# Optimization experiments

Hardware: AMD Instinct MI355X
Metric: run time of the kernel (lower is better)

Reference implementation:

```python
import jax, jax.numpy as jnp
import numpy as np

B, S, E, H = 4, 2048, 1024, 16
Dh = E // H
EPS = 1e-5


def setup_inputs() -> dict:
    key = jax.random.key(0)
    ks = jax.random.split(key, 16)
    w = lambda k, shp: jax.random.normal(k, shp, dtype=jnp.float32) * 0.02
    return {
        "x": jax.random.normal(ks[0], (B, S, E), dtype=jnp.float32),
        "Wq": w(ks[1], (E, E)), "bq": jnp.zeros((E,), jnp.float32),
        "Wk": w(ks[2], (E, E)), "bk": jnp.zeros((E,), jnp.float32),
        "Wv": w(ks[3], (E, E)), "bv": jnp.zeros((E,), jnp.float32),
        "Wo": w(ks[4], (E, E)), "bo": jnp.zeros((E,), jnp.float32),
        "an1_a": jnp.ones((1, S, 1), jnp.float32),
        "an1_b": jnp.zeros((1, S, 1), jnp.float32),
        "W1": w(ks[5], (2 * E, E)), "b1": jnp.zeros((2 * E,), jnp.float32),
        "W2": w(ks[6], (E, 2 * E)), "b2": jnp.zeros((E,), jnp.float32),
        "an2_a": jnp.ones((1, S, 1), jnp.float32),
        "an2_b": jnp.zeros((1, S, 1), jnp.float32),
    }


def adaptive_norm(x, a, b):
    # AdaptiveNorm((1, N_s, 1)): normalize over embedding dim, per-position affine.
    mu = jnp.mean(x, axis=-1, keepdims=True)
    var = jnp.mean(jnp.square(x - mu), axis=-1, keepdims=True)
    return a * (x - mu) * jax.lax.rsqrt(var + EPS) + b


def reference(x, Wq, bq, Wk, bk, Wv, bv, Wo, bo, an1_a, an1_b, W1, b1, W2, b2, an2_a, an2_b):
    scale = 1.0 / np.sqrt(E / H)
    # QKV projections -> (B, S, H, Dh)
    q = (x @ Wq.T + bq).reshape(B, S, H, Dh)
    k = (x @ Wk.T + bk).reshape(B, S, H, Dh)
    v = (x @ Wv.T + bv).reshape(B, S, H, Dh)
    # scaled dot-product attention (materializes B,H,S,S like the original)
    scores = jnp.einsum("bshd,bthd->bhst", q, k) * scale
    probs = jax.nn.softmax(scores, axis=-1)
    attn = jnp.einsum("bhst,bthd->bshd", probs, v).reshape(B, S, E)
    attn = attn @ Wo.T + bo
    # residual + adaptive norm (dropout is identity in eval mode)
    h = adaptive_norm(attn + x, an1_a, an1_b)
    ff = jax.nn.relu(h @ W1.T + b1) @ W2.T + b2
    out = adaptive_norm(ff + h, an2_a, an2_b)
    return out
```

## Files before the change

kernel.cpp:

```cpp
#include <hip/hip_runtime.h>


typedef __attribute__((ext_vector_type(8))) short s16x8;
typedef __attribute__((ext_vector_type(4))) short s16x4;
typedef __attribute__((ext_vector_type(4))) unsigned short u16x4;
typedef __attribute__((ext_vector_type(4))) float f32x4;

__device__ __forceinline__ float bf2f(unsigned short u) {
  unsigned int v = ((unsigned int)u) << 16;
  return __builtin_bit_cast(float, v);
}
__device__ __forceinline__ unsigned short f2bf(float f) {
  unsigned int u = __builtin_bit_cast(unsigned int, f);
  u += 0x7fffu + ((u >> 16) & 1u);
  return (unsigned short)(u >> 16);
}
__device__ __forceinline__ unsigned int pkbf_trunc(float f0, float f1) {
  return __builtin_amdgcn_perm(__builtin_bit_cast(unsigned int, f1),
                               __builtin_bit_cast(unsigned int, f0), 0x07060302u);
}
__device__ __forceinline__ f32x4 mfma16(s16x8 a, s16x8 b, f32x4 c) {
  return __builtin_amdgcn_mfma_f32_16x16x32_bf16(a, b, c, 0, 0, 0);
}
__device__ __forceinline__ void gl2lds16(const unsigned short* g, unsigned short* l) {
  __builtin_amdgcn_global_load_lds(
      (const __attribute__((address_space(1))) unsigned int*)(g),
      (__attribute__((address_space(3))) unsigned int*)(l), 16, 0, 0);
}

__global__ void detect_dtype(const unsigned int* __restrict__ x, int* __restrict__ flag) {
  const int tid = threadIdx.x;
  int cnt = 0;
  for (int i = tid; i < 2048; i += 256) {
    const unsigned e = (x[i] >> 7) & 0xFF;
    cnt += (e >= 100 && e <= 150) ? 1 : 0;
  }
#pragma unroll
  for (int off = 32; off >= 1; off >>= 1) cnt += __shfl_xor(cnt, off);
  __shared__ int red[4];
  if ((tid & 63) == 0) red[tid >> 6] = cnt;
  __syncthreads();
  if (tid == 0) *flag = ((red[0] + red[1] + red[2] + red[3]) > 1536) ? 1 : 0;
}

struct CvtArgs {
  const void* src[17];
  unsigned short* dst[17];
  int cum4[18];
};

__global__ __launch_bounds__(256) void cvt_all(CvtArgs a, const int* __restrict__ flag, int total4) {
  const int i = blockIdx.x * 256 + threadIdx.x;
  if (i >= total4) return;
  int lo = 0, hi = 17;
  while (hi - lo > 1) {
    const int mid = (lo + hi) >> 1;
    if (i >= a.cum4[mid]) lo = mid; else hi = mid;
  }
  const int off4 = i - a.cum4[lo];
  if (*flag) {
    const u16x4* s = (const u16x4*)a.src[lo];
    *(u16x4*)&a.dst[lo][off4 * 4] = s[off4];
  } else {
    const float4* s = (const float4*)a.src[lo];
    const float4 v = s[off4];
    u16x4 o;
    o[0] = f2bf(v.x); o[1] = f2bf(v.y); o[2] = f2bf(v.z); o[3] = f2bf(v.w);
    *(u16x4*)&a.dst[lo][off4 * 4] = o;
  }
}

#define BM 128
#define BN 128
#define BKK 64
#define QOFF 8388608L
#define SCALE2 0.18033688011f

template <int EPI>
__global__ __launch_bounds__(256, 2) void gemm_bt(
    const unsigned short* __restrict__ A, const unsigned short* __restrict__ W,
    const unsigned short* __restrict__ bias, const unsigned short* __restrict__ resid,
    unsigned short* __restrict__ out, int M, int N, int K) {
  __shared__ unsigned short Al[BM * BKK];
  __shared__ unsigned short Bl[BN * BKK];
  const int tid = threadIdx.x;
  const int lane = tid & 63;
  const int wave = tid >> 6;
  const int qd = lane >> 4;
  const int c = lane & 15;
  const int wm = (wave >> 1) * 64;
  const int wn = (wave & 1) * 64;
  const long m0 = (long)blockIdx.y * BM;
  const long n0 = (long)blockIdx.x * BN;

  f32x4 acc[4][4] = {};

  const int scc = ((tid & 7) ^ ((tid >> 3) & 7)) * 8;
  const unsigned short* Ag = A + (m0 + (tid >> 3)) * (long)K + scc;
  const unsigned short* Wg = W + (n0 + (tid >> 3)) * (long)K + scc;

  for (int k0 = 0; k0 < K; k0 += BKK) {
    __syncthreads();
#pragma unroll
    for (int p = 0; p < 4; ++p)
      gl2lds16(Ag + (long)p * 32 * K + k0, &Al[(p * 256 + tid) * 8]);
#pragma unroll
    for (int p = 0; p < 4; ++p)
      gl2lds16(Wg + (long)p * 32 * K + k0, &Bl[(p * 256 + tid) * 8]);
    __syncthreads();
#pragma unroll
    for (int ks = 0; ks < 2; ++ks) {
      const int ch = ((ks * 4 + qd) ^ (c & 7)) * 8;
      s16x8 af[4], bfr[4];
#pragma unroll
      for (int mt = 0; mt < 4; ++mt)
        af[mt] = *(const s16x8*)&Al[(wm + mt * 16 + c) * BKK + ch];
#pragma unroll
      for (int nt = 0; nt < 4; ++nt)
        bfr[nt] = *(const s16x8*)&Bl[(wn + nt * 16 + c) * BKK + ch];
#pragma unroll
      for (int mt = 0; mt < 4; ++mt)
#pragma unroll
        for (int nt = 0; nt < 4; ++nt)
          acc[mt][nt] = mfma16(af[mt], bfr[nt], acc[mt][nt]);
    }
  }

#pragma unroll
  for (int nt = 0; nt < 4; ++nt) {
    const int gn = (int)n0 + wn + nt * 16 + c;
    const float bv = bf2f(bias[gn]);
#pragma unroll
    for (int mt = 0; mt < 4; ++mt) {
      const long gmb = m0 + wm + mt * 16 + qd * 4;
      if constexpr (EPI == 2) {
#pragma unroll
        for (int r = 0; r < 4; ++r) {
          const long gm = gmb + r;
          const float v = acc[mt][nt][r] + bv + bf2f(resid[gm * N + gn]);
          out[gm * N + gn] = f2bf(v);
        }
      } else if constexpr (EPI == 3) {
#pragma unroll
        for (int r = 0; r < 4; ++r) {
          const long gm = gmb + r;
          float v = acc[mt][nt][r] + bv;
          v = fmaxf(v, 0.0f);
          out[gm * N + gn] = f2bf(v);
        }
      } else {
        const int seg = gn >> 10;
        const int nn = gn & 1023;
        if (seg == 0) {
#pragma unroll
          for (int r = 0; r < 4; ++r)
            out[(gmb + r) * 1024 + nn] = f2bf((acc[mt][nt][r] + bv) * SCALE2);
        } else if (seg == 1) {
#pragma unroll
          for (int r = 0; r < 4; ++r)
            (out + QOFF)[(gmb + r) * 1024 + nn] = f2bf(acc[mt][nt][r] + bv);
        } else {
          const int h = nn >> 6, d = nn & 63;
          const long b = gmb >> 11;
          const int s = (int)(gmb & 2047);
          s16x4 pv;
#pragma unroll
          for (int r = 0; r < 4; ++r) pv[r] = (short)f2bf(acc[mt][nt][r] + bv);
          *(s16x4*)&(out + 2 * QOFF)[((b * 16 + h) * 64L + d) * 2048 + s] = pv;
        }
      }
    }
  }
}

#define ATT_S 2048

__global__ __launch_bounds__(256)
__attribute__((amdgpu_waves_per_eu(2, 2))) void attn_fwd(
    const unsigned short* __restrict__ Q, const unsigned short* __restrict__ K,
    const unsigned short* __restrict__ VT, unsigned short* __restrict__ O) {
  __shared__ unsigned short SH[24576];
  unsigned short* Kb0 = SH;
  unsigned short* Kb1 = SH + 4096;
  unsigned short* Vb0 = SH + 8192;
  unsigned short* Vb1 = SH + 12288;
  unsigned short* Pl  = SH + 16384;

  const int bh = blockIdx.y;
  const int q0 = blockIdx.x * 256;
  const long b = bh >> 4;
  const int h = bh & 15;
  const unsigned short* Qg = Q + (b * 2048) * 1024 + h * 64;
  const unsigned short* Kg = K + (b * 2048) * 1024 + h * 64;
  const unsigned short* Vg = VT + (long)bh * 64 * 2048;

  const int tid = threadIdx.x;
  const int wave = tid >> 6, lane = tid & 63;
  const int qd = lane >> 4, c = lane & 15;
  const int mb = wave * 32;

  const int srow = tid >> 3;
  const int sccs = ((tid & 7) ^ (srow & 7)) * 8;

  s16x8 qf[2][2][2];
#pragma unroll
  for (int h2 = 0; h2 < 2; ++h2)
#pragma unroll
    for (int mt = 0; mt < 2; ++mt)
#pragma unroll
      for (int ks = 0; ks < 2; ++ks)
        qf[h2][mt][ks] = *(const s16x8*)&Qg[(long)(q0 + h2 * 128 + mb + mt * 16 + c) * 1024 +
                                            ks * 32 + qd * 8];

  s16x8 ones;
#pragma unroll
  for (int i = 0; i < 8; ++i) ones[i] = (short)0x3F80;

  f32x4 oacc[2][4][2] = {};
  f32x4 lacc[2][2] = {};

  gl2lds16(Kg + (long)srow * 1024 + sccs, &Kb0[tid * 8]);
  gl2lds16(Kg + (long)(srow + 32) * 1024 + sccs, &Kb0[(256 + tid) * 8]);
  gl2lds16(Vg + (long)srow * 2048 + sccs, &Vb0[tid * 8]);
  gl2lds16(Vg + (long)(srow + 32) * 2048 + sccs, &Vb0[(256 + tid) * 8]);

  for (int it = 0; it < 32; ++it) {
    const int p = it & 1;
    unsigned short* Kc = p ? Kb1 : Kb0;
    unsigned short* Vc = p ? Vb1 : Vb0;
    unsigned short* Kn = p ? Kb0 : Kb1;
    unsigned short* Vn = p ? Vb0 : Vb1;
    const int kvn = (it < 31) ? (it + 1) * 64 : 31 * 64;
    gl2lds16(Kg + (long)(kvn + srow) * 1024 + sccs, &Kn[tid * 8]);
    gl2lds16(Kg + (long)(kvn + srow + 32) * 1024 + sccs, &Kn[(256 + tid) * 8]);
    gl2lds16(Vg + (long)srow * 2048 + kvn + sccs, &Vn[tid * 8]);
    gl2lds16(Vg + (long)(srow + 32) * 2048 + kvn + sccs, &Vn[(256 + tid) * 8]);

    asm volatile("s_waitcnt vmcnt(4)\n\ts_barrier" ::: "memory");

#pragma unroll
    for (int h2 = 0; h2 < 2; ++h2) {
      f32x4 sacc[4][2] = {};
#pragma unroll
      for (int ks = 0; ks < 2; ++ks) {
        const int ch = ((ks * 4 + qd) ^ (c & 7)) * 8;
        s16x8 kf[4];
#pragma unroll
        for (int tt = 0; tt < 4; ++tt)
          kf[tt] = *(const s16x8*)&Kc[(tt * 16 + c) * 64 + ch];
#pragma unroll
        for (int mt = 0; mt < 2; ++mt)
#pragma unroll
          for (int tt = 0; tt < 4; ++tt)
            sacc[tt][mt] = mfma16(kf[tt], qf[h2][mt][ks], sacc[tt][mt]);
      }

#pragma unroll
      for (int mt = 0; mt < 2; ++mt) {
        const int ml = mb + mt * 16 + c;
#pragma unroll
        for (int tt = 0; tt < 4; ++tt) {
          unsigned int pk[2];
          pk[0] = pkbf_trunc(__builtin_amdgcn_exp2f(sacc[tt][mt][0]),
                             __builtin_amdgcn_exp2f(sacc[tt][mt][1]));
          pk[1] = pkbf_trunc(__builtin_amdgcn_exp2f(sacc[tt][mt][2]),
                             __builtin_amdgcn_exp2f(sacc[tt][mt][3]));
          const int chw = ((tt * 2 + (qd >> 1)) ^ (ml & 7)) * 8 + (qd & 1) * 4;
          *(uint2*)&Pl[ml * 64 + chw] = *(uint2*)pk;
        }
      }
      asm volatile("s_waitcnt lgkmcnt(0)" ::: "memory");

#pragma unroll
      for (int ks = 0; ks < 2; ++ks) {
        const int vch = ((ks * 4 + qd) ^ (c & 7)) * 8;
        s16x8 vf[4], pf[2];
#pragma unroll
        for (int dt = 0; dt < 4; ++dt)
          vf[dt] = *(const s16x8*)&Vc[(dt * 16 + c) * 64 + vch];
#pragma unroll
        for (int mt = 0; mt < 2; ++mt) {
          const int pr = mb + mt * 16 + c;
          pf[mt] = *(const s16x8*)&Pl[pr * 64 + (((ks * 4 + qd) ^ (pr & 7)) * 8)];
        }
#pragma unroll
        for (int mt = 0; mt < 2; ++mt) {
#pragma unroll
          for (int dt = 0; dt < 4; ++dt)
            oacc[h2][dt][mt] = mfma16(vf[dt], pf[mt], oacc[h2][dt][mt]);
          lacc[h2][mt] = mfma16(ones, pf[mt], lacc[h2][mt]);
        }
      }
    }

    asm volatile("s_barrier" ::: "memory");
  }

#pragma unroll
  for (int h2 = 0; h2 < 2; ++h2)
#pragma unroll
    for (int mt = 0; mt < 2; ++mt) {
      const float inv = 1.0f / lacc[h2][mt][0];
      const int s = q0 + h2 * 128 + mb + mt * 16 + c;
      const long ob = (b * (long)ATT_S + s) * 1024L + h * 64;
#pragma unroll
      for (int dt = 0; dt < 4; ++dt) {
        s16x4 ov;
#pragma unroll
        for (int r = 0; r < 4; ++r) ov[r] = (short)f2bf(oacc[h2][dt][mt][r] * inv);
        *(s16x4*)&O[ob + dt * 16 + qd * 4] = ov;
      }
    }
}

template <bool FINAL>
__global__ __launch_bounds__(256) void norm_affine(
    const unsigned short* __restrict__ X, const unsigned short* __restrict__ av,
    const unsigned short* __restrict__ bv, void* __restrict__ outv,
    const int* __restrict__ flag) {
  const int row = blockIdx.x;
  const int s = row & 2047;
  const unsigned short* xr = X + (long)row * 1024;
  const int tid = threadIdx.x;
  const u16x4 u = *(const u16x4*)&xr[tid * 4];
  float v[4];
  float s1 = 0.f, s2 = 0.f;
#pragma unroll
  for (int i = 0; i < 4; ++i) {
    v[i] = bf2f(u[i]);
    s1 += v[i];
    s2 += v[i] * v[i];
  }
#pragma unroll
  for (int off = 32; off >= 1; off >>= 1) {
    s1 += __shfl_xor(s1, off);
    s2 += __shfl_xor(s2, off);
  }
  __shared__ float red[8];
  const int wave = tid >> 6, lane = tid & 63;
  if (lane == 0) {
    red[wave * 2] = s1;
    red[wave * 2 + 1] = s2;
  }
  __syncthreads();
  s1 = red[0] + red[2] + red[4] + red[6];
  s2 = red[1] + red[3] + red[5] + red[7];
  const float mean = s1 * (1.0f / 1024.0f);
  const float var = fmaxf(s2 * (1.0f / 1024.0f) - mean * mean, 0.0f);
  const float rstd = rsqrtf(var + 1e-5f);
  const float aa = bf2f(av[s]), bb = bf2f(bv[s]);
  float o[4];
#pragma unroll
  for (int i = 0; i < 4; ++i) o[i] = aa * (v[i] - mean) * rstd + bb;
  bool as_bf16 = true;
  if constexpr (FINAL) as_bf16 = (*flag != 0);
  if (as_bf16) {
    u16x4 ob;
#pragma unroll
    for (int i = 0; i < 4; ++i) ob[i] = f2bf(o[i]);
    *(u16x4*)&((unsigned short*)outv)[(long)row * 1024 + tid * 4] = ob;
  } else {
    float4 of = {o[0], o[1], o[2], o[3]};
    *(float4*)&((float*)outv)[(long)row * 1024 + tid * 4] = of;
  }
}

extern "C" void kernel_launch(void* const* d_in, const int* in_sizes, int n_in,
                              void* d_out, int out_size, void* d_ws, size_t ws_size,
                              hipStream_t stream) {
  char* ws = (char*)d_ws;
  const size_t SZ = 8192ull * 1024 * 2;
  const size_t WSZ = 1024ull * 1024 * 2;

  unsigned short* xb   = (unsigned short*)(ws);
  unsigned short* qb   = (unsigned short*)(ws + SZ);
  unsigned short* kb   = (unsigned short*)(ws + 2 * SZ);
  unsigned short* vtb  = (unsigned short*)(ws + 3 * SZ);
  unsigned short* attn = (unsigned short*)(ws + 4 * SZ);
  unsigned short* hb   = (unsigned short*)(ws + 5 * SZ);
  unsigned short* r1   = qb;
  unsigned short* ffb  = kb;
  unsigned short* r2   = attn;

  char* wreg = ws + 6 * SZ;
  unsigned short* wqb = (unsigned short*)(wreg);
  unsigned short* w1b = (unsigned short*)(wreg + 4 * WSZ);
  unsigned short* w2b = (unsigned short*)(wreg + 6 * WSZ);
  unsigned short* wob = (unsigned short*)(wreg + 3 * WSZ);
  unsigned short* smal = (unsigned short*)(wreg + 8 * WSZ);
  unsigned short* bqb = smal;
  unsigned short* bkb = smal + 1024;
  unsigned short* bvb = smal + 2048;
  unsigned short* bob = smal + 3072;
  unsigned short* b1b = smal + 4096;
  unsigned short* b2b = smal + 6144;
  unsigned short* a1b = smal + 7168;
  unsigned short* g1b = smal + 9216;
  unsigned short* a2b = smal + 11264;
  unsigned short* g2b = smal + 13312;
  int* flag = (int*)(wreg + 8 * WSZ + 64 * 1024);

  CvtArgs ca;
  unsigned short* wkb = wqb + 1024 * 1024;
  unsigned short* wvb = wqb + 2 * 1024 * 1024;
  unsigned short* dsts[17] = {xb, wqb, bqb, wkb, bkb, wvb, bvb, wob, bob,
                              a1b, g1b, w1b, b1b, w2b, b2b, a2b, g2b};
  ca.cum4[0] = 0;
  for (int i = 0; i < 17; ++i) {
    ca.src[i] = d_in[i];
    ca.dst[i] = dsts[i];
    ca.cum4[i + 1] = ca.cum4[i] + in_sizes[i] / 4;
  }
  const int total4 = ca.cum4[17];

  dim3 blk(256);
  detect_dtype<<<1, blk, 0, stream>>>((const unsigned int*)d_in[0], flag);
  cvt_all<<<(total4 + 255) / 256, blk, 0, stream>>>(ca, flag, total4);

  gemm_bt<4><<<dim3(24, 64), blk, 0, stream>>>(xb, wqb, bqb, nullptr, qb, 8192, 3072, 1024);
  attn_fwd<<<dim3(8, 64), blk, 0, stream>>>(qb, kb, vtb, attn);
  gemm_bt<2><<<dim3(8, 64), blk, 0, stream>>>(attn, wob, bob, xb, r1, 8192, 1024, 1024);
  norm_affine<false><<<8192, blk, 0, stream>>>(r1, a1b, g1b, hb, nullptr);
  gemm_bt<3><<<dim3(16, 64), blk, 0, stream>>>(hb, w1b, b1b, nullptr, ffb, 8192, 2048, 1024);
  gemm_bt<2><<<dim3(8, 64), blk, 0, stream>>>(ffb, w2b, b2b, hb, r2, 8192, 1024, 2048);
  norm_affine<true><<<8192, blk, 0, stream>>>(r2, a2b, g2b, d_out, flag);
}
```

Measured before the change: 435.7 us.

## Rewrite GEMM as 8-wave 256x128 tile with triple-buffered async LDS pipeline

Result: faster. 421.0 us (-3.4%).

```diff
diff --git a/kernel.cpp b/kernel.cpp
--- a/kernel.cpp
+++ b/kernel.cpp
@@ -70,69 +70,101 @@
   }
 }
 
-#define BM 128
-#define BN 128
-#define BKK 64
 #define QOFF 8388608L
 #define SCALE2 0.18033688011f
 
 template <int EPI>
-__global__ __launch_bounds__(256, 2) void gemm_bt(
+__global__ __launch_bounds__(512, 1) void gemm8(
     const unsigned short* __restrict__ A, const unsigned short* __restrict__ W,
     const unsigned short* __restrict__ bias, const unsigned short* __restrict__ resid,
     unsigned short* __restrict__ out, int M, int N, int K) {
-  __shared__ unsigned short Al[BM * BKK];
-  __shared__ unsigned short Bl[BN * BKK];
+  extern __shared__ unsigned short sh[];
   const int tid = threadIdx.x;
   const int lane = tid & 63;
   const int wave = tid >> 6;
   const int qd = lane >> 4;
   const int c = lane & 15;
-  const int wm = (wave >> 1) * 64;
-  const int wn = (wave & 1) * 64;
-  const long m0 = (long)blockIdx.y * BM;
-  const long n0 = (long)blockIdx.x * BN;
-
-  f32x4 acc[4][4] = {};
-
-  const int scc = ((tid & 7) ^ ((tid >> 3) & 7)) * 8;
-  const unsigned short* Ag = A + (m0 + (tid >> 3)) * (long)K + scc;
-  const unsigned short* Wg = W + (n0 + (tid >> 3)) * (long)K + scc;
-
-  for (int k0 = 0; k0 < K; k0 += BKK) {
-    __syncthreads();
-#pragma unroll
-    for (int p = 0; p < 4; ++p)
-      gl2lds16(Ag + (long)p * 32 * K + k0, &Al[(p * 256 + tid) * 8]);
-#pragma unroll
-    for (int p = 0; p < 4; ++p)
-      gl2lds16(Wg + (long)p * 32 * K + k0, &Bl[(p * 256 + tid) * 8]);
-    __syncthreads();
-#pragma unroll
-    for (int ks = 0; ks < 2; ++ks) {
-      const int ch = ((ks * 4 + qd) ^ (c & 7)) * 8;
-      s16x8 af[4], bfr[4];
-#pragma unroll
-      for (int mt = 0; mt < 4; ++mt)
-        af[mt] = *(const s16x8*)&Al[(wm + mt * 16 + c) * BKK + ch];
-#pragma unroll
-      for (int nt = 0; nt < 4; ++nt)
-        bfr[nt] = *(const s16x8*)&Bl[(wn + nt * 16 + c) * BKK + ch];
-#pragma unroll
-      for (int mt = 0; mt < 4; ++mt)
-#pragma unroll
-        for (int nt = 0; nt < 4; ++nt)
+  const int wr128 = (wave >> 2) * 128;
+  const int wc32 = (wave & 3) * 32;
+  const long m0 = (long)blockIdx.y * 256;
+  const long n0 = (long)blockIdx.x * 128;
+
+  const int srow = tid >> 3;
+  const int scc = ((tid & 7) ^ (srow & 7)) * 8;
+  const unsigned short* Asrc = A + (m0 + srow) * (long)K + scc;
+  const unsigned short* Wsrc = W + (n0 + srow) * (long)K + scc;
+  const int lofs = tid * 8;
+
+  f32x4 acc[8][2] = {};
+
+#pragma unroll
+  for (int q = 0; q < 4; ++q) gl2lds16(Asrc + (long)q * 64 * K, sh + q * 4096 + lofs);
+#pragma unroll
+  for (int q = 0; q < 2; ++q) gl2lds16(Wsrc + (long)q * 64 * K, sh + 16384 + q * 4096 + lofs);
+#pragma unroll
+  for (int q = 0; q < 4; ++q)
+    gl2lds16(Asrc + (long)q * 64 * K + 64, sh + 24576 + q * 4096 + lofs);
+#pragma unroll
+  for (int q = 0; q < 2; ++q)
+    gl2lds16(Wsrc + (long)q * 64 * K + 64, sh + 24576 + 16384 + q * 4096 + lofs);
+
+  const int NT = K >> 6;
+  int cur = 0;
+  for (int t = 0; t < NT; ++t) {
+    if (t == NT - 1)
+      asm volatile("s_waitcnt vmcnt(0)\n\ts_barrier" ::: "memory");
+    else
+      asm volatile("s_waitcnt vmcnt(6)\n\ts_barrier" ::: "memory");
+
+    const unsigned short* Ac = sh + cur * 24576;
+    const unsigned short* Bc = Ac + 16384;
+    const int nxt = (cur + 2 >= 3) ? cur - 1 : cur + 2;
+    unsigned short* An = sh + nxt * 24576;
+    unsigned short* Bn = An + 16384;
+    const bool do_stage = (t + 2 < NT);
+    const long kt = (long)(t + 2) * 64;
+
+#pragma unroll
+    for (int ph = 0; ph < 2; ++ph) {
+      const int ch = ((ph * 4 + qd) ^ (c & 7)) * 8;
+      s16x8 af[8], bfr[2];
+#pragma unroll
+      for (int mt = 0; mt < 8; ++mt)
+        af[mt] = *(const s16x8*)&Ac[(wr128 + mt * 16 + c) * 64 + ch];
+#pragma unroll
+      for (int nt = 0; nt < 2; ++nt)
+        bfr[nt] = *(const s16x8*)&Bc[(wc32 + nt * 16 + c) * 64 + ch];
+      if (do_stage) {
+        if (ph == 0) {
+          gl2lds16(Asrc + kt, An + lofs);
+          gl2lds16(Asrc + (long)64 * K + kt, An + 4096 + lofs);
+          gl2lds16(Asrc + (long)128 * K + kt, An + 8192 + lofs);
+        } else {
+          gl2lds16(Asrc + (long)192 * K + kt, An + 12288 + lofs);
+          gl2lds16(Wsrc + kt, Bn + lofs);
+          gl2lds16(Wsrc + (long)64 * K + kt, Bn + 4096 + lofs);
+        }
+      }
+      asm volatile("s_barrier" ::: "memory");
+      __builtin_amdgcn_s_setprio(1);
+#pragma unroll
+      for (int mt = 0; mt < 8; ++mt)
+#pragma unroll
+        for (int nt = 0; nt < 2; ++nt)
           acc[mt][nt] = mfma16(af[mt], bfr[nt], acc[mt][nt]);
+      __builtin_amdgcn_s_setprio(0);
+      if (ph == 0) asm volatile("s_barrier" ::: "memory");
     }
-  }
-
-#pragma unroll
-  for (int nt = 0; nt < 4; ++nt) {
-    const int gn = (int)n0 + wn + nt * 16 + c;
+    cur = (cur + 1 == 3) ? 0 : cur + 1;
+  }
+
+#pragma unroll
+  for (int nt = 0; nt < 2; ++nt) {
+    const int gn = (int)n0 + wc32 + nt * 16 + c;
     const float bv = bf2f(bias[gn]);
 #pragma unroll
-    for (int mt = 0; mt < 4; ++mt) {
-      const long gmb = m0 + wm + mt * 16 + qd * 4;
+    for (int mt = 0; mt < 8; ++mt) {
+      const long gmb = m0 + wr128 + mt * 16 + qd * 4;
       if constexpr (EPI == 2) {
 #pragma unroll
         for (int r = 0; r < 4; ++r) {
@@ -413,15 +445,28 @@
   }
   const int total4 = ca.cum4[17];
 
+  static bool attr_set = false;
+  if (!attr_set) {
+    attr_set = true;
+    hipFuncSetAttribute(reinterpret_cast<const void*>(gemm8<2>),
+                        hipFuncAttributeMaxDynamicSharedMemorySize, 147456);
+    hipFuncSetAttribute(reinterpret_cast<const void*>(gemm8<3>),
+                        hipFuncAttributeMaxDynamicSharedMemorySize, 147456);
+    hipFuncSetAttribute(reinterpret_cast<const void*>(gemm8<4>),
+                        hipFuncAttributeMaxDynamicSharedMemorySize, 147456);
+  }
+
   dim3 blk(256);
+  dim3 blk512(512);
+  const int GLDS = 147456;
   detect_dtype<<<1, blk, 0, stream>>>((const unsigned int*)d_in[0], flag);
   cvt_all<<<(total4 + 255) / 256, blk, 0, stream>>>(ca, flag, total4);
 
-  gemm_bt<4><<<dim3(24, 64), blk, 0, stream>>>(xb, wqb, bqb, nullptr, qb, 8192, 3072, 1024);
+  gemm8<4><<<dim3(24, 32), blk512, GLDS, stream>>>(xb, wqb, bqb, nullptr, qb, 8192, 3072, 1024);
   attn_fwd<<<dim3(8, 64), blk, 0, stream>>>(qb, kb, vtb, attn);
-  gemm_bt<2><<<dim3(8, 64), blk, 0, stream>>>(attn, wob, bob, xb, r1, 8192, 1024, 1024);
+  gemm8<2><<<dim3(8, 32), blk512, GLDS, stream>>>(attn, wob, bob, xb, r1, 8192, 1024, 1024);
   norm_affine<false><<<8192, blk, 0, stream>>>(r1, a1b, g1b, hb, nullptr);
-  gemm_bt<3><<<dim3(16, 64), blk, 0, stream>>>(hb, w1b, b1b, nullptr, ffb, 8192, 2048, 1024);
-  gemm_bt<2><<<dim3(8, 64), blk, 0, stream>>>(ffb, w2b, b2b, hb, r2, 8192, 1024, 2048);
+  gemm8<3><<<dim3(16, 32), blk512, GLDS, stream>>>(hb, w1b, b1b, nullptr, ffb, 8192, 2048, 1024);
+  gemm8<2><<<dim3(8, 32), blk512, GLDS, stream>>>(ffb, w2b, b2b, hb, r2, 8192, 1024, 2048);
   norm_affine<true><<<8192, blk, 0, stream>>>(r2, a2b, g2b, d_out, flag);
 }
```

## Replace GEMM with 512-thread multi-stage pipelined kernel using larger tiles

Applied to the files above, without the earlier changes.

Result: no change. 435.6 us (-0.0%).

```diff
diff --git a/kernel.cpp b/kernel.cpp
--- a/kernel.cpp
+++ b/kernel.cpp
@@ -70,69 +70,111 @@
   }
 }
 
-#define BM 128
-#define BN 128
-#define BKK 64
 #define QOFF 8388608L
 #define SCALE2 0.18033688011f
 
-template <int EPI>
-__global__ __launch_bounds__(256, 2) void gemm_bt(
+template <int EPI, int BM>
+__global__ __launch_bounds__(512, 1) void gemmP(
     const unsigned short* __restrict__ A, const unsigned short* __restrict__ W,
     const unsigned short* __restrict__ bias, const unsigned short* __restrict__ resid,
     unsigned short* __restrict__ out, int M, int N, int K) {
-  __shared__ unsigned short Al[BM * BKK];
-  __shared__ unsigned short Bl[BN * BKK];
+  constexpr int BN = 256;
+  constexpr int TS = (BM + BN) * 32;
+  constexpr int LD = (BM + BN) / 128;
+  constexpr int NPH = BM / 128;
+  extern __shared__ unsigned short sh[];
+
   const int tid = threadIdx.x;
   const int lane = tid & 63;
   const int wave = tid >> 6;
   const int qd = lane >> 4;
   const int c = lane & 15;
-  const int wm = (wave >> 1) * 64;
-  const int wn = (wave & 1) * 64;
+  const int wr = (wave >> 2) * (BM / 2);
+  const int wc = (wave & 3) * 64;
   const long m0 = (long)blockIdx.y * BM;
   const long n0 = (long)blockIdx.x * BN;
 
-  f32x4 acc[4][4] = {};
-
-  const int scc = ((tid & 7) ^ ((tid >> 3) & 7)) * 8;
-  const unsigned short* Ag = A + (m0 + (tid >> 3)) * (long)K + scc;
-  const unsigned short* Wg = W + (n0 + (tid >> 3)) * (long)K + scc;
-
-  for (int k0 = 0; k0 < K; k0 += BKK) {
-    __syncthreads();
-#pragma unroll
-    for (int p = 0; p < 4; ++p)
-      gl2lds16(Ag + (long)p * 32 * K + k0, &Al[(p * 256 + tid) * 8]);
-#pragma unroll
-    for (int p = 0; p < 4; ++p)
-      gl2lds16(Wg + (long)p * 32 * K + k0, &Bl[(p * 256 + tid) * 8]);
-    __syncthreads();
-#pragma unroll
-    for (int ks = 0; ks < 2; ++ks) {
-      const int ch = ((ks * 4 + qd) ^ (c & 7)) * 8;
-      s16x8 af[4], bfr[4];
+  const int srow = tid >> 2;
+  const int scol = (tid & 3) * 8;
+  const unsigned short* Asrc = A + (m0 + srow) * (long)K + scol;
+  const unsigned short* Wsrc = W + (n0 + srow) * (long)K + scol;
+
+  f32x4 acc[NPH * 4][4] = {};
+
+  const int NT = K >> 5;
+
+  auto stage = [&](int tt, int part) {
+    unsigned short* dst = sh + (tt & 3) * TS;
+    const long kof = (long)tt * 32;
+    if (part < BM / 128) {
+      gl2lds16(Asrc + (long)part * 128 * K + kof, dst + part * 4096 + tid * 8);
+    } else {
+      const int bp = part - BM / 128;
+      gl2lds16(Wsrc + (long)bp * 128 * K + kof, dst + BM * 32 + bp * 4096 + tid * 8);
+    }
+  };
+
+#pragma unroll
+  for (int tt = 0; tt < 3; ++tt)
+#pragma unroll
+    for (int p = 0; p < LD; ++p) stage(tt, p);
+
+  for (int t = 0; t < NT; ++t) {
+    if (t + 2 < NT) {
+      if constexpr (BM == 256) asm volatile("s_waitcnt vmcnt(8)" ::: "memory");
+      else                     asm volatile("s_waitcnt vmcnt(6)" ::: "memory");
+    } else if (t + 1 < NT) {
+      if constexpr (BM == 256) asm volatile("s_waitcnt vmcnt(4)" ::: "memory");
+      else                     asm volatile("s_waitcnt vmcnt(3)" ::: "memory");
+    } else {
+      asm volatile("s_waitcnt vmcnt(0)" ::: "memory");
+    }
+    asm volatile("s_barrier" ::: "memory");
+
+    const unsigned short* Ab = sh + (t & 3) * TS;
+    const unsigned short* Bb = Ab + BM * 32;
+    const bool dost = (t + 3 < NT);
+
+    s16x8 bf[4];
+#pragma unroll
+    for (int nt = 0; nt < 4; ++nt)
+      bf[nt] = *(const s16x8*)&Bb[(wc + nt * 16 + c) * 32 + qd * 8];
+
+#pragma unroll
+    for (int ph = 0; ph < NPH; ++ph) {
+      s16x8 af[4];
 #pragma unroll
       for (int mt = 0; mt < 4; ++mt)
-        af[mt] = *(const s16x8*)&Al[(wm + mt * 16 + c) * BKK + ch];
-#pragma unroll
-      for (int nt = 0; nt < 4; ++nt)
-        bfr[nt] = *(const s16x8*)&Bl[(wn + nt * 16 + c) * BKK + ch];
+        af[mt] = *(const s16x8*)&Ab[(wr + ph * 64 + mt * 16 + c) * 32 + qd * 8];
+      if (dost) {
+        if constexpr (BM == 256) {
+          stage(t + 3, ph * 2 + 0);
+          stage(t + 3, ph * 2 + 1);
+        } else {
+          stage(t + 3, 0);
+          stage(t + 3, 1);
+          stage(t + 3, 2);
+        }
+      }
+      asm volatile("s_barrier" ::: "memory");
+      __builtin_amdgcn_s_setprio(1);
 #pragma unroll
       for (int mt = 0; mt < 4; ++mt)
 #pragma unroll
         for (int nt = 0; nt < 4; ++nt)
-          acc[mt][nt] = mfma16(af[mt], bfr[nt], acc[mt][nt]);
+          acc[ph * 4 + mt][nt] = mfma16(af[mt], bf[nt], acc[ph * 4 + mt][nt]);
+      __builtin_amdgcn_s_setprio(0);
+      if (ph + 1 < NPH) asm volatile("s_barrier" ::: "memory");
     }
   }
 
 #pragma unroll
   for (int nt = 0; nt < 4; ++nt) {
-    const int gn = (int)n0 + wn + nt * 16 + c;
+    const int gn = (int)n0 + wc + nt * 16 + c;
     const float bv = bf2f(bias[gn]);
 #pragma unroll
-    for (int mt = 0; mt < 4; ++mt) {
-      const long gmb = m0 + wm + mt * 16 + qd * 4;
+    for (int mt = 0; mt < NPH * 4; ++mt) {
+      const long gmb = m0 + wr + mt * 16 + qd * 4;
       if constexpr (EPI == 2) {
 #pragma unroll
         for (int r = 0; r < 4; ++r) {
@@ -413,15 +455,27 @@
   }
   const int total4 = ca.cum4[17];
 
+  static bool attr_set = false;
+  if (!attr_set) {
+    attr_set = true;
+    hipFuncSetAttribute(reinterpret_cast<const void*>(gemmP<4, 128>),
+                        hipFuncAttributeMaxDynamicSharedMemorySize, 98304);
+    hipFuncSetAttribute(reinterpret_cast<const void*>(gemmP<2, 128>),
+                        hipFuncAttributeMaxDynamicSharedMemorySize, 98304);
+    hipFuncSetAttribute(reinterpret_cast<const void*>(gemmP<3, 256>),
+                        hipFuncAttributeMaxDynamicSharedMemorySize, 131072);
+  }
+
   dim3 blk(256);
+  dim3 blk512(512);
   detect_dtype<<<1, blk, 0, stream>>>((const unsigned int*)d_in[0], flag);
   cvt_all<<<(total4 + 255) / 256, blk, 0, stream>>>(ca, flag, total4);
 
-  gemm_bt<4><<<dim3(24, 64), blk, 0, stream>>>(xb, wqb, bqb, nullptr, qb, 8192, 3072, 1024);
+  gemmP<4, 128><<<dim3(12, 64), blk512, 98304, stream>>>(xb, wqb, bqb, nullptr, qb, 8192, 3072, 1024);
   attn_fwd<<<dim3(8, 64), blk, 0, stream>>>(qb, kb, vtb, attn);
-  gemm_bt<2><<<dim3(8, 64), blk, 0, stream>>>(attn, wob, bob, xb, r1, 8192, 1024, 1024);
+  gemmP<2, 128><<<dim3(4, 64), blk512, 98304, stream>>>(attn, wob, bob, xb, r1, 8192, 1024, 1024);
   norm_affine<false><<<8192, blk, 0, stream>>>(r1, a1b, g1b, hb, nullptr);
-  gemm_bt<3><<<dim3(16, 64), blk, 0, stream>>>(hb, w1b, b1b, nullptr, ffb, 8192, 2048, 1024);
-  gemm_bt<2><<<dim3(8, 64), blk, 0, stream>>>(ffb, w2b, b2b, hb, r2, 8192, 1024, 2048);
+  gemmP<3, 256><<<dim3(8, 32), blk512, 131072, stream>>>(hb, w1b, b1b, nullptr, ffb, 8192, 2048, 1024);
+  gemmP<2, 128><<<dim3(4, 64), blk512, 98304, stream>>>(ffb, w2b, b2b, hb, r2, 8192, 1024, 2048);
   norm_affine<true><<<8192, blk, 0, stream>>>(r2, a2b, g2b, d_out, flag);
 }
```

## Rewrite GEMM as 256x256 double-buffered pipelined kernel with XCD-aware block remap

Applied to the files above, without the earlier changes.

Measured after the change: 458.9 us. 5.3% more time.

```diff
diff --git a/kernel.cpp b/kernel.cpp
--- a/kernel.cpp
+++ b/kernel.cpp
@@ -70,69 +70,110 @@
   }
 }
 
-#define BM 128
-#define BN 128
-#define BKK 64
 #define QOFF 8388608L
 #define SCALE2 0.18033688011f
 
 template <int EPI>
-__global__ __launch_bounds__(256, 2) void gemm_bt(
+__global__ __launch_bounds__(512, 1) void gemm2(
     const unsigned short* __restrict__ A, const unsigned short* __restrict__ W,
     const unsigned short* __restrict__ bias, const unsigned short* __restrict__ resid,
     unsigned short* __restrict__ out, int M, int N, int K) {
-  __shared__ unsigned short Al[BM * BKK];
-  __shared__ unsigned short Bl[BN * BKK];
+  extern __shared__ unsigned short sh[];
+
   const int tid = threadIdx.x;
   const int lane = tid & 63;
   const int wave = tid >> 6;
   const int qd = lane >> 4;
   const int c = lane & 15;
-  const int wm = (wave >> 1) * 64;
-  const int wn = (wave & 1) * 64;
-  const long m0 = (long)blockIdx.y * BM;
-  const long n0 = (long)blockIdx.x * BN;
-
-  f32x4 acc[4][4] = {};
-
-  const int scc = ((tid & 7) ^ ((tid >> 3) & 7)) * 8;
-  const unsigned short* Ag = A + (m0 + (tid >> 3)) * (long)K + scc;
-  const unsigned short* Wg = W + (n0 + (tid >> 3)) * (long)K + scc;
-
-  for (int k0 = 0; k0 < K; k0 += BKK) {
-    __syncthreads();
-#pragma unroll
-    for (int p = 0; p < 4; ++p)
-      gl2lds16(Ag + (long)p * 32 * K + k0, &Al[(p * 256 + tid) * 8]);
-#pragma unroll
-    for (int p = 0; p < 4; ++p)
-      gl2lds16(Wg + (long)p * 32 * K + k0, &Bl[(p * 256 + tid) * 8]);
-    __syncthreads();
-#pragma unroll
-    for (int ks = 0; ks < 2; ++ks) {
-      const int ch = ((ks * 4 + qd) ^ (c & 7)) * 8;
-      s16x8 af[4], bfr[4];
+  const int wr = (wave >> 2) * 128;
+  const int wc = (wave & 3) * 64;
+
+  const int nx = gridDim.x, ny = gridDim.y;
+  const int nwg = nx * ny;
+  int lin = blockIdx.y * nx + blockIdx.x;
+  lin = (lin & 7) * (nwg >> 3) + (lin >> 3);
+  const int by = lin % ny;
+  const int bx = lin / ny;
+  const long m0 = (long)by * 256;
+  const long n0 = (long)bx * 256;
+
+  const int srow = tid >> 3;
+  const int scc = ((tid & 7) ^ (srow & 7)) * 8;
+  const unsigned short* Asrc = A + (m0 + srow) * (long)K + scc;
+  const unsigned short* Wsrc = W + (n0 + srow) * (long)K + scc;
+  const int lofs = tid * 8;
+
+  f32x4 acc[8][4] = {};
+
+  const int NT = K >> 6;
+
+  auto stageA = [&](int tt, int q) {
+    gl2lds16(Asrc + (long)q * 64 * K + (long)tt * 64,
+             sh + (tt & 1) * 32768 + q * 4096 + lofs);
+  };
+  auto stageB = [&](int tt, int q) {
+    gl2lds16(Wsrc + (long)q * 64 * K + (long)tt * 64,
+             sh + (tt & 1) * 32768 + 16384 + q * 4096 + lofs);
+  };
+
+  stageB(0, 0); stageB(0, 1); stageB(0, 2); stageB(0, 3);
+  stageA(0, 0); stageA(0, 2); stageA(0, 1); stageA(0, 3);
+
+  for (int t = 0; t < NT; ++t) {
+    const unsigned short* Ab = sh + (t & 1) * 32768;
+    const unsigned short* Bb = Ab + 16384;
+    const bool dost = (t + 1 < NT);
+
+#pragma unroll
+    for (int ph = 0; ph < 4; ++ph) {
+      const int qm = ph >> 1, qn = ph & 1;
+      if (ph == 0)
+        asm volatile("s_waitcnt vmcnt(2)\n\ts_barrier" ::: "memory");
+      else if (ph == 2) {
+        if (dost) asm volatile("s_waitcnt vmcnt(6)\n\ts_barrier" ::: "memory");
+        else      asm volatile("s_waitcnt vmcnt(0)\n\ts_barrier" ::: "memory");
+      } else
+        asm volatile("s_barrier" ::: "memory");
+
+      s16x8 af[4][2], bfr[2][2];
+#pragma unroll
+      for (int ks = 0; ks < 2; ++ks) {
+#pragma unroll
+        for (int mt = 0; mt < 4; ++mt)
+          af[mt][ks] = *(const s16x8*)&Ab[(wr + qm * 64 + mt * 16 + c) * 64 +
+                                          (((ks * 4 + qd) ^ (c & 7)) * 8)];
+#pragma unroll
+        for (int nt = 0; nt < 2; ++nt)
+          bfr[nt][ks] = *(const s16x8*)&Bb[(wc + qn * 32 + nt * 16 + c) * 64 +
+                                           (((ks * 4 + qd) ^ (c & 7)) * 8)];
+      }
+
+      if (dost) {
+        if (ph == 0) { stageB(t + 1, 0); stageB(t + 1, 1); stageB(t + 1, 2); stageB(t + 1, 3); }
+        else if (ph == 1) { stageA(t + 1, 0); stageA(t + 1, 2); }
+        else if (ph == 2) { stageA(t + 1, 1); stageA(t + 1, 3); }
+      }
+
+      __builtin_amdgcn_s_setprio(1);
 #pragma unroll
       for (int mt = 0; mt < 4; ++mt)
-        af[mt] = *(const s16x8*)&Al[(wm + mt * 16 + c) * BKK + ch];
-#pragma unroll
-      for (int nt = 0; nt < 4; ++nt)
-        bfr[nt] = *(const s16x8*)&Bl[(wn + nt * 16 + c) * BKK + ch];
-#pragma unroll
-      for (int mt = 0; mt < 4; ++mt)
-#pragma unroll
-        for (int nt = 0; nt < 4; ++nt)
-          acc[mt][nt] = mfma16(af[mt], bfr[nt], acc[mt][nt]);
+#pragma unroll
+        for (int nt = 0; nt < 2; ++nt)
+#pragma unroll
+          for (int ks = 0; ks < 2; ++ks)
+            acc[qm * 4 + mt][qn * 2 + nt] =
+                mfma16(af[mt][ks], bfr[nt][ks], acc[qm * 4 + mt][qn * 2 + nt]);
+      __builtin_amdgcn_s_setprio(0);
     }
   }
 
 #pragma unroll
   for (int nt = 0; nt < 4; ++nt) {
-    const int gn = (int)n0 + wn + nt * 16 + c;
+    const int gn = (int)n0 + wc + nt * 16 + c;
     const float bv = bf2f(bias[gn]);
 #pragma unroll
-    for (int mt = 0; mt < 4; ++mt) {
-      const long gmb = m0 + wm + mt * 16 + qd * 4;
+    for (int mt = 0; mt < 8; ++mt) {
+      const long gmb = m0 + wr + mt * 16 + qd * 4;
       if constexpr (EPI == 2) {
 #pragma unroll
         for (int r = 0; r < 4; ++r) {
@@ -413,15 +454,28 @@
   }
   const int total4 = ca.cum4[17];
 
+  static bool attr_set = false;
+  if (!attr_set) {
+    attr_set = true;
+    hipFuncSetAttribute(reinterpret_cast<const void*>(gemm2<2>),
+                        hipFuncAttributeMaxDynamicSharedMemorySize, 131072);
+    hipFuncSetAttribute(reinterpret_cast<const void*>(gemm2<3>),
+                        hipFuncAttributeMaxDynamicSharedMemorySize, 131072);
+    hipFuncSetAttribute(reinterpret_cast<const void*>(gemm2<4>),
+                        hipFuncAttributeMaxDynamicSharedMemorySize, 131072);
+  }
+
   dim3 blk(256);
+  dim3 blk512(512);
+  const int GLDS = 131072;
   detect_dtype<<<1, blk, 0, stream>>>((const unsigned int*)d_in[0], flag);
   cvt_all<<<(total4 + 255) / 256, blk, 0, stream>>>(ca, flag, total4);
 
-  gemm_bt<4><<<dim3(24, 64), blk, 0, stream>>>(xb, wqb, bqb, nullptr, qb, 8192, 3072, 1024);
+  gemm2<4><<<dim3(12, 32), blk512, GLDS, stream>>>(xb, wqb, bqb, nullptr, qb, 8192, 3072, 1024);
   attn_fwd<<<dim3(8, 64), blk, 0, stream>>>(qb, kb, vtb, attn);
-  gemm_bt<2><<<dim3(8, 64), blk, 0, stream>>>(attn, wob, bob, xb, r1, 8192, 1024, 1024);
+  gemm2<2><<<dim3(4, 32), blk512, GLDS, stream>>>(attn, wob, bob, xb, r1, 8192, 1024, 1024);
   norm_affine<false><<<8192, blk, 0, stream>>>(r1, a1b, g1b, hb, nullptr);
-  gemm_bt<3><<<dim3(16, 64), blk, 0, stream>>>(hb, w1b, b1b, nullptr, ffb, 8192, 2048, 1024);
-  gemm_bt<2><<<dim3(8, 64), blk, 0, stream>>>(ffb, w2b, b2b, hb, r2, 8192, 1024, 2048);
+  gemm2<3><<<dim3(8, 32), blk512, GLDS, stream>>>(hb, w1b, b1b, nullptr, ffb, 8192, 2048, 1024);
+  gemm2<2><<<dim3(4, 32), blk512, GLDS, stream>>>(ffb, w2b, b2b, hb, r2, 8192, 1024, 2048);
   norm_affine<true><<<8192, blk, 0, stream>>>(r2, a2b, g2b, d_out, flag);
 }
```
